# Kernel optimization log

Measured on AMD Instinct MI355X. Metric: run time of the kernel, lower is better.

## Reference

```python
import jax, jax.numpy as jnp
import numpy as np


def setup_inputs() -> dict:
    key = jax.random.key(0)
    k1, k2, k3, k4, k5, k6 = jax.random.split(key, 6)
    B, N, C, H = 4096, 64, 192, 6
    NW = 64  # windows per image; must divide B
    TABLE = 225  # (2*8-1)**2
    qkv = jax.random.normal(k1, (B, N, 3 * C), dtype=jnp.float32)
    rpi = jax.random.randint(k2, (N, N), 0, TABLE, dtype=jnp.int64)
    mask = jax.random.normal(k3, (NW, N, N), dtype=jnp.float32)
    rpb_table = jax.random.normal(k4, (TABLE, H), dtype=jnp.float32) * 0.02
    proj_w = jax.random.normal(k5, (C, C), dtype=jnp.float32) * 0.02
    proj_b = jax.random.normal(k6, (C,), dtype=jnp.float32) * 0.02
    return {"qkv": qkv, "rpi": rpi, "mask": mask, "rpb_table": rpb_table,
            "proj_w": proj_w, "proj_b": proj_b}


def reference(qkv, rpi, mask, rpb_table, proj_w, proj_b):
    b_, n, c3 = qkv.shape
    c = c3 // 3
    h = rpb_table.shape[1]           # num_heads
    hd = c // h                      # head_dim
    scale = hd ** (-0.5)
    # (b_, n, 3, h, hd) -> (3, b_, h, n, hd)
    qkv = qkv.reshape(b_, n, 3, h, hd).transpose(2, 0, 3, 1, 4)
    q, k, v = qkv[0] * scale, qkv[1], qkv[2]
    # windowed QK^T: [b_, h, n, n]
    attn = jnp.einsum('bhqd,bhkd->bhqk', q, k)
    # relative position bias gather: rpi [n,n] -> [h,n,n]
    bias = rpb_table[rpi].transpose(2, 0, 1)
    attn = attn + bias[None]
    # shift-window mask add
    nw = mask.shape[0]
    attn = attn.reshape(b_ // nw, nw, h, n, n) + mask[None, :, None]
    attn = attn.reshape(b_, h, n, n)
    attn = jax.nn.softmax(attn, axis=-1)
    # AV then output projection
    out = jnp.einsum('bhqk,bhkd->bhqd', attn, v)
    out = out.transpose(0, 2, 1, 3).reshape(b_, n, c)
    return out @ proj_w.T + proj_b
```

## Files before the change

kernel.cpp:

```cpp
#include <hip/hip_runtime.h>
#include <stdint.h>

typedef __bf16 bf16x8 __attribute__((ext_vector_type(8)));
typedef float f32x4 __attribute__((ext_vector_type(4)));

__device__ __forceinline__ unsigned short f2bf(float f) {
    union { __bf16 h; unsigned short u; } v;
    v.h = (__bf16)f;
    return v.u;
}
__device__ __forceinline__ float bf2f(unsigned short u) {
    union { uint32_t u32; float f; } v;
    v.u32 = ((uint32_t)u) << 16;
    return v.f;
}

#define QS_STRIDE 40
#define VT_STRIDE 72
#define PS_STRIDE 72
#define XS_STRIDE 200

__global__ void prep_all(const int* __restrict__ rpi32,
                         const float* __restrict__ rpb,
                         const float* __restrict__ proj_w,
                         unsigned short* __restrict__ rpbT,
                         unsigned short* __restrict__ wf) {
    int bid = blockIdx.x;
    int tid = threadIdx.x;
    if (bid < 96) {
        __shared__ int is64_s;
        if (tid == 0) {
            int s = 0;
            #pragma unroll
            for (int i = 0; i < 16; ++i) s |= rpi32[2 * i + 1];
            is64_s = (s == 0);
        }
        __syncthreads();
        int g = bid * 256 + tid;
        int e = g & 4095;
        int h = g >> 12;
        int rv = is64_s ? rpi32[2 * e] : rpi32[e];
        rpbT[g] = f2bf(rpb[rv * 6 + h]);
    } else {
        int g = (bid - 96) * 256 + tid;
        int e = g & 7;
        int lane = (g >> 3) & 63;
        int kkct = g >> 9;
        int kk = kkct / 12, ct = kkct % 12;
        int co = ct * 16 + (lane & 15);
        int ki = kk * 32 + (lane >> 4) * 8 + e;
        wf[g] = f2bf(proj_w[co * 192 + ki]);
    }
}


__global__ __launch_bounds__(256, 3)
void winattn_fast(const float* __restrict__ qkv,
                  const float* __restrict__ mask,
                  const unsigned short* __restrict__ rpbT,
                  const unsigned short* __restrict__ wf,
                  const float* __restrict__ proj_b,
                  float* __restrict__ out) {
    __shared__ __align__(16) unsigned short x_s[64 * XS_STRIDE];
    __shared__ __align__(16) unsigned short u_s[7424];
    __shared__ __align__(16) unsigned short p_s[4 * 16 * PS_STRIDE];

    unsigned short* q_s  = u_s;
    unsigned short* k_s  = u_s + 2560;
    unsigned short* vT_s = u_s + 5120;

    const int tid  = threadIdx.x;
    const int b    = blockIdx.x;
    const int lane = tid & 63;
    const int wv   = tid >> 6;
    const int l16  = lane & 15;
    const int lhi  = lane >> 4;
    const int qbase = wv * 16;
    const float scale = 0.17677669529663687f;

    const float* qkv_b = qkv + (size_t)b * 64 * 576;
    const float* mask_l = mask + (size_t)(b & 63) * 4096 + (qbase + l16) * 64 + lhi * 4;
    const unsigned short* rpb_l = rpbT + (qbase + l16) * 64 + lhi * 4;

    const int tokA = tid >> 3;
    const int dA   = (tid & 7) << 2;
    const float4* gA = (const float4*)(qkv_b + tokA * 576 + dA);
    const float4* gB = (const float4*)(qkv_b + (tokA + 32) * 576 + dA);

    float4 q0, k0, v0, q1, k1, v1;

#define LOADH(h_)  do { int o = (h_) * 8;                         \
        q0 = gA[o];      k0 = gA[o + 48]; v0 = gA[o + 96];        \
        q1 = gB[o];      k1 = gB[o + 48]; v1 = gB[o + 96]; } while (0)

#define STOREH() do {                                             \
        ushort4 qh, kh;                                           \
        qh.x = f2bf(q0.x * scale); qh.y = f2bf(q0.y * scale);     \
        qh.z = f2bf(q0.z * scale); qh.w = f2bf(q0.w * scale);     \
        kh.x = f2bf(k0.x); kh.y = f2bf(k0.y);                     \
        kh.z = f2bf(k0.z); kh.w = f2bf(k0.w);                     \
        *(ushort4*)&q_s[tokA * QS_STRIDE + dA] = qh;              \
        *(ushort4*)&k_s[tokA * QS_STRIDE + dA] = kh;              \
        vT_s[(dA + 0) * VT_STRIDE + tokA] = f2bf(v0.x);           \
        vT_s[(dA + 1) * VT_STRIDE + tokA] = f2bf(v0.y);           \
        vT_s[(dA + 2) * VT_STRIDE + tokA] = f2bf(v0.z);           \
        vT_s[(dA + 3) * VT_STRIDE + tokA] = f2bf(v0.w);           \
        qh.x = f2bf(q1.x * scale); qh.y = f2bf(q1.y * scale);     \
        qh.z = f2bf(q1.z * scale); qh.w = f2bf(q1.w * scale);     \
        kh.x = f2bf(k1.x); kh.y = f2bf(k1.y);                     \
        kh.z = f2bf(k1.z); kh.w = f2bf(k1.w);                     \
        *(ushort4*)&q_s[(tokA + 32) * QS_STRIDE + dA] = qh;       \
        *(ushort4*)&k_s[(tokA + 32) * QS_STRIDE + dA] = kh;       \
        vT_s[(dA + 0) * VT_STRIDE + tokA + 32] = f2bf(v1.x);      \
        vT_s[(dA + 1) * VT_STRIDE + tokA + 32] = f2bf(v1.y);      \
        vT_s[(dA + 2) * VT_STRIDE + tokA + 32] = f2bf(v1.z);      \
        vT_s[(dA + 3) * VT_STRIDE + tokA + 32] = f2bf(v1.w); } while (0)

    LOADH(0);
    STOREH();

    unsigned short* pw = p_s + wv * 16 * PS_STRIDE;

    float4 mv[4];
    #pragma unroll
    for (int nt = 0; nt < 4; ++nt)
        mv[nt] = *(const float4*)&mask_l[nt * 16];
    ushort4 rb[4], rbn[4];
    #pragma unroll
    for (int nt = 0; nt < 4; ++nt)
        rb[nt] = *(const ushort4*)&rpb_l[nt * 16];

    for (int h = 0; h < 6; ++h) {
        __syncthreads();
        if (h < 5) {
            LOADH(h + 1);
            #pragma unroll
            for (int nt = 0; nt < 4; ++nt)
                rbn[nt] = *(const ushort4*)&rpb_l[(h + 1) * 4096 + nt * 16];
        }

        float bias[4][4];
        #pragma unroll
        for (int nt = 0; nt < 4; ++nt) {
            bias[nt][0] = mv[nt].x + bf2f(rb[nt].x);
            bias[nt][1] = mv[nt].y + bf2f(rb[nt].y);
            bias[nt][2] = mv[nt].z + bf2f(rb[nt].z);
            bias[nt][3] = mv[nt].w + bf2f(rb[nt].w);
        }

        bf16x8 aq = *(const bf16x8*)&q_s[(qbase + l16) * QS_STRIDE + lhi * 8];
        float lg[4][4];
        #pragma unroll
        for (int nt = 0; nt < 4; ++nt) {
            bf16x8 bk = *(const bf16x8*)&k_s[(nt * 16 + l16) * QS_STRIDE + lhi * 8];
            f32x4 c = {0.f, 0.f, 0.f, 0.f};
            c = __builtin_amdgcn_mfma_f32_16x16x32_bf16(bk, aq, c, 0, 0, 0);
            lg[nt][0] = c[0] + bias[nt][0]; lg[nt][1] = c[1] + bias[nt][1];
            lg[nt][2] = c[2] + bias[nt][2]; lg[nt][3] = c[3] + bias[nt][3];
        }

        float m = lg[0][0];
        #pragma unroll
        for (int nt = 0; nt < 4; ++nt)
            #pragma unroll
            for (int j = 0; j < 4; ++j) m = fmaxf(m, lg[nt][j]);
        m = fmaxf(m, __shfl_xor(m, 16, 64));
        m = fmaxf(m, __shfl_xor(m, 32, 64));
        float s = 0.f;
        #pragma unroll
        for (int nt = 0; nt < 4; ++nt)
            #pragma unroll
            for (int j = 0; j < 4; ++j) { lg[nt][j] = __expf(lg[nt][j] - m); s += lg[nt][j]; }
        s += __shfl_xor(s, 16, 64);
        s += __shfl_xor(s, 32, 64);
        float inv = __builtin_amdgcn_rcpf(s);

        #pragma unroll
        for (int nt = 0; nt < 4; ++nt) {
            ushort4 ph;
            ph.x = f2bf(lg[nt][0] * inv); ph.y = f2bf(lg[nt][1] * inv);
            ph.z = f2bf(lg[nt][2] * inv); ph.w = f2bf(lg[nt][3] * inv);
            *(ushort4*)&pw[l16 * PS_STRIDE + nt * 16 + lhi * 4] = ph;
        }

        f32x4 xo[2] = {{0.f,0.f,0.f,0.f},{0.f,0.f,0.f,0.f}};
        #pragma unroll
        for (int kk = 0; kk < 2; ++kk) {
            bf16x8 pa = *(const bf16x8*)&pw[l16 * PS_STRIDE + kk * 32 + lhi * 8];
            #pragma unroll
            for (int dt = 0; dt < 2; ++dt) {
                bf16x8 vb = *(const bf16x8*)&vT_s[(dt * 16 + l16) * VT_STRIDE + kk * 32 + lhi * 8];
                xo[dt] = __builtin_amdgcn_mfma_f32_16x16x32_bf16(pa, vb, xo[dt], 0, 0, 0);
            }
        }
        #pragma unroll
        for (int j = 0; j < 4; ++j) {
            int n = qbase + lhi * 4 + j;
            #pragma unroll
            for (int dt = 0; dt < 2; ++dt)
                x_s[n * XS_STRIDE + h * 32 + dt * 16 + l16] = f2bf(xo[dt][j]);
        }

        __syncthreads();
        if (h < 5) {
            STOREH();
            #pragma unroll
            for (int nt = 0; nt < 4; ++nt) rb[nt] = rbn[nt];
        }
    }
#undef LOADH
#undef STOREH

    f32x4 oacc[12];
    #pragma unroll
    for (int ct = 0; ct < 12; ++ct) oacc[ct] = (f32x4){0.f, 0.f, 0.f, 0.f};
    #pragma unroll
    for (int kk = 0; kk < 6; ++kk) {
        bf16x8 ax = *(const bf16x8*)&x_s[(qbase + l16) * XS_STRIDE + kk * 32 + lhi * 8];
        #pragma unroll
        for (int ct = 0; ct < 12; ++ct) {
            bf16x8 bw = *(const bf16x8*)&wf[((kk * 12 + ct) * 64 + lane) * 8];
            oacc[ct] = __builtin_amdgcn_mfma_f32_16x16x32_bf16(ax, bw, oacc[ct], 0, 0, 0);
        }
    }
    float* outb = out + (size_t)b * 64 * 192;
    #pragma unroll
    for (int ct = 0; ct < 12; ++ct) {
        int co = ct * 16 + l16;
        float bias = proj_b[co];
        #pragma unroll
        for (int j = 0; j < 4; ++j) {
            int n = qbase + lhi * 4 + j;
            outb[n * 192 + co] = oacc[ct][j] + bias;
        }
    }
}


#define WS_STRIDE 40

__global__ __launch_bounds__(256)
void winattn_fused(const float* __restrict__ qkv,
                   const int* __restrict__ rpi32,
                   const float* __restrict__ mask,
                   const float* __restrict__ rpb_table,
                   const float* __restrict__ proj_w,
                   const float* __restrict__ proj_b,
                   float* __restrict__ out) {
    __shared__ __align__(16) unsigned short x_s[64 * XS_STRIDE];
    __shared__ __align__(16) unsigned short u_s[12032];
    __shared__ float rpb_s[225];
    __shared__ int rpi_is64_s;

    unsigned short* q_s  = u_s;
    unsigned short* k_s  = u_s + 2560;
    unsigned short* vT_s = u_s + 5120;
    unsigned short* p_s  = u_s + 7424;
    unsigned short* w_s  = u_s;

    const int tid  = threadIdx.x;
    const int b    = blockIdx.x;
    const int lane = tid & 63;
    const int wv   = tid >> 6;
    const int l16  = lane & 15;
    const int lhi  = lane >> 4;
    const int qbase = wv * 16;
    const float scale = 0.17677669529663687f;

    if (tid == 0) {
        int s = 0;
        #pragma unroll
        for (int i = 0; i < 16; ++i) s |= rpi32[2 * i + 1];
        rpi_is64_s = (s == 0) ? 1 : 0;
    }

    const float* maskw = mask + (size_t)(b & 63) * 4096;
    const float* qkv_b = qkv + (size_t)b * 64 * 576;

    for (int h = 0; h < 6; ++h) {
        for (int idx = tid; idx < 64 * 8; idx += 256) {
            int tok = idx >> 3, d = (idx & 7) << 2;
            const float4* base = (const float4*)(qkv_b + tok * 576 + h * 32 + d);
            float4 qv = base[0];
            float4 kv = base[48];
            float4 vv = base[96];
            ushort4 qh, kh;
            qh.x = f2bf(qv.x * scale); qh.y = f2bf(qv.y * scale);
            qh.z = f2bf(qv.z * scale); qh.w = f2bf(qv.w * scale);
            kh.x = f2bf(kv.x); kh.y = f2bf(kv.y); kh.z = f2bf(kv.z); kh.w = f2bf(kv.w);
            *(ushort4*)&q_s[tok * QS_STRIDE + d] = qh;
            *(ushort4*)&k_s[tok * QS_STRIDE + d] = kh;
            vT_s[(d + 0) * VT_STRIDE + tok] = f2bf(vv.x);
            vT_s[(d + 1) * VT_STRIDE + tok] = f2bf(vv.y);
            vT_s[(d + 2) * VT_STRIDE + tok] = f2bf(vv.z);
            vT_s[(d + 3) * VT_STRIDE + tok] = f2bf(vv.w);
        }
        if (tid < 225) rpb_s[tid] = rpb_table[tid * 6 + h];
        __syncthreads();
        const int is64 = rpi_is64_s;

        bf16x8 aq = *(const bf16x8*)&q_s[(qbase + l16) * QS_STRIDE + lhi * 8];
        float lg[4][4];
        #pragma unroll
        for (int nt = 0; nt < 4; ++nt) {
            bf16x8 bk = *(const bf16x8*)&k_s[(nt * 16 + l16) * QS_STRIDE + lhi * 8];
            f32x4 c = {0.f, 0.f, 0.f, 0.f};
            c = __builtin_amdgcn_mfma_f32_16x16x32_bf16(aq, bk, c, 0, 0, 0);
            #pragma unroll
            for (int j = 0; j < 4; ++j) lg[nt][j] = c[j];
        }
        #pragma unroll
        for (int nt = 0; nt < 4; ++nt) {
            int c = nt * 16 + l16;
            #pragma unroll
            for (int j = 0; j < 4; ++j) {
                int r = qbase + lhi * 4 + j;
                int e = r * 64 + c;
                int rv = is64 ? rpi32[2 * e] : rpi32[e];
                lg[nt][j] += rpb_s[rv] + maskw[e];
            }
        }
        float srow[4];
        float p[4][4];
        #pragma unroll
        for (int j = 0; j < 4; ++j) {
            float m = fmaxf(fmaxf(lg[0][j], lg[1][j]), fmaxf(lg[2][j], lg[3][j]));
            #pragma unroll
            for (int o = 1; o < 16; o <<= 1) m = fmaxf(m, __shfl_xor(m, o, 64));
            float s = 0.f;
            #pragma unroll
            for (int nt = 0; nt < 4; ++nt) { p[nt][j] = __expf(lg[nt][j] - m); s += p[nt][j]; }
            #pragma unroll
            for (int o = 1; o < 16; o <<= 1) s += __shfl_xor(s, o, 64);
            srow[j] = s;
        }
        __syncthreads();
        unsigned short* pw = p_s + wv * 16 * PS_STRIDE;
        #pragma unroll
        for (int nt = 0; nt < 4; ++nt)
            #pragma unroll
            for (int j = 0; j < 4; ++j)
                pw[(lhi * 4 + j) * PS_STRIDE + nt * 16 + l16] = f2bf(p[nt][j]);
        __syncthreads();

        f32x4 xo[2] = {{0.f,0.f,0.f,0.f},{0.f,0.f,0.f,0.f}};
        #pragma unroll
        for (int kk = 0; kk < 2; ++kk) {
            bf16x8 pa = *(const bf16x8*)&pw[l16 * PS_STRIDE + kk * 32 + lhi * 8];
            #pragma unroll
            for (int dt = 0; dt < 2; ++dt) {
                bf16x8 vb = *(const bf16x8*)&vT_s[(dt * 16 + l16) * VT_STRIDE + kk * 32 + lhi * 8];
                xo[dt] = __builtin_amdgcn_mfma_f32_16x16x32_bf16(pa, vb, xo[dt], 0, 0, 0);
            }
        }
        #pragma unroll
        for (int j = 0; j < 4; ++j) {
            float inv = 1.f / srow[j];
            int n = qbase + lhi * 4 + j;
            #pragma unroll
            for (int dt = 0; dt < 2; ++dt)
                x_s[n * XS_STRIDE + h * 32 + dt * 16 + l16] = f2bf(xo[dt][j] * inv);
        }
        __syncthreads();
    }

    f32x4 oacc[12];
    #pragma unroll
    for (int ct = 0; ct < 12; ++ct) oacc[ct] = (f32x4){0.f, 0.f, 0.f, 0.f};
    for (int kk = 0; kk < 6; ++kk) {
        for (int idx = tid; idx < 192 * 8; idx += 256) {
            int co = idx >> 3, d = (idx & 7) << 2;
            float4 wvv = *(const float4*)(proj_w + co * 192 + kk * 32 + d);
            ushort4 wh;
            wh.x = f2bf(wvv.x); wh.y = f2bf(wvv.y); wh.z = f2bf(wvv.z); wh.w = f2bf(wvv.w);
            *(ushort4*)&w_s[co * WS_STRIDE + d] = wh;
        }
        __syncthreads();
        bf16x8 ax = *(const bf16x8*)&x_s[(qbase + l16) * XS_STRIDE + kk * 32 + lhi * 8];
        #pragma unroll
        for (int ct = 0; ct < 12; ++ct) {
            bf16x8 bw = *(const bf16x8*)&w_s[(ct * 16 + l16) * WS_STRIDE + lhi * 8];
            oacc[ct] = __builtin_amdgcn_mfma_f32_16x16x32_bf16(ax, bw, oacc[ct], 0, 0, 0);
        }
        __syncthreads();
    }
    float* outb = out + (size_t)b * 64 * 192;
    #pragma unroll
    for (int ct = 0; ct < 12; ++ct) {
        int co = ct * 16 + l16;
        float bias = proj_b[co];
        #pragma unroll
        for (int j = 0; j < 4; ++j) {
            int n = qbase + lhi * 4 + j;
            outb[n * 192 + co] = oacc[ct][j] + bias;
        }
    }
}

extern "C" void kernel_launch(void* const* d_in, const int* in_sizes, int n_in,
                              void* d_out, int out_size, void* d_ws, size_t ws_size,
                              hipStream_t stream) {
    (void)in_sizes; (void)n_in; (void)out_size;
    const float* qkv       = (const float*)d_in[0];
    const int*   rpi       = (const int*)d_in[1];
    const float* mask      = (const float*)d_in[2];
    const float* rpb_table = (const float*)d_in[3];
    const float* proj_w    = (const float*)d_in[4];
    const float* proj_b    = (const float*)d_in[5];
    float* out = (float*)d_out;

    const size_t RT_BYTES = (size_t)6 * 4096 * sizeof(unsigned short);
    const size_t WF_BYTES = (size_t)36864 * sizeof(unsigned short);

    if (ws_size >= RT_BYTES + WF_BYTES) {
        unsigned short* rpbT = (unsigned short*)d_ws;
        unsigned short* wfp  = (unsigned short*)((char*)d_ws + RT_BYTES);
        prep_all<<<240, 256, 0, stream>>>(rpi, rpb_table, proj_w, rpbT, wfp);
        winattn_fast<<<4096, 256, 0, stream>>>(qkv, mask, rpbT, wfp, proj_b, out);
    } else {
        winattn_fused<<<4096, 256, 0, stream>>>(qkv, rpi, mask, rpb_table, proj_w, proj_b, out);
    }
}
```

Measured before the change: 186.7 us.

## Double-buffer per-head QKV tiles and keep attention outputs in registers

The per-head q/k/vT shared tile is now double-buffered. That removes the second __syncthreads per head, and the global load for head h+2 is issued one iteration earlier. The full 64x192 bf16 x_s staging buffer is replaced by a small per-wave 16x32 scratch. Each head's A-fragment for the output projection is read back right away and held in six bf16x8 registers. This lowers LDS footprint and barrier count, at the cost of more live registers under launch_bounds(256,3).

```diff
diff --git a/kernel.cpp b/kernel.cpp
--- a/kernel.cpp
+++ b/kernel.cpp
@@ -18,7 +18,7 @@
 #define QS_STRIDE 40
 #define VT_STRIDE 72
 #define PS_STRIDE 72
-#define XS_STRIDE 200
+#define XH_STRIDE 40
 
 __global__ void prep_all(const int* __restrict__ rpi32,
                          const float* __restrict__ rpb,
@@ -61,13 +61,9 @@
                   const unsigned short* __restrict__ wf,
                   const float* __restrict__ proj_b,
                   float* __restrict__ out) {
-    __shared__ __align__(16) unsigned short x_s[64 * XS_STRIDE];
-    __shared__ __align__(16) unsigned short u_s[7424];
+    __shared__ __align__(16) unsigned short u_s[2][7424];
     __shared__ __align__(16) unsigned short p_s[4 * 16 * PS_STRIDE];
-
-    unsigned short* q_s  = u_s;
-    unsigned short* k_s  = u_s + 2560;
-    unsigned short* vT_s = u_s + 5120;
+    __shared__ __align__(16) unsigned short xh_s[4 * 16 * XH_STRIDE];
 
     const int tid  = threadIdx.x;
     const int b    = blockIdx.x;
@@ -93,33 +89,38 @@
         q0 = gA[o];      k0 = gA[o + 48]; v0 = gA[o + 96];        \
         q1 = gB[o];      k1 = gB[o + 48]; v1 = gB[o + 96]; } while (0)
 
-#define STOREH() do {                                             \
+#define STOREH(buf) do {                                          \
+        unsigned short* q_w  = (buf);                             \
+        unsigned short* k_w  = (buf) + 2560;                      \
+        unsigned short* vT_w = (buf) + 5120;                      \
         ushort4 qh, kh;                                           \
         qh.x = f2bf(q0.x * scale); qh.y = f2bf(q0.y * scale);     \
         qh.z = f2bf(q0.z * scale); qh.w = f2bf(q0.w * scale);     \
         kh.x = f2bf(k0.x); kh.y = f2bf(k0.y);                     \
         kh.z = f2bf(k0.z); kh.w = f2bf(k0.w);                     \
-        *(ushort4*)&q_s[tokA * QS_STRIDE + dA] = qh;              \
-        *(ushort4*)&k_s[tokA * QS_STRIDE + dA] = kh;              \
-        vT_s[(dA + 0) * VT_STRIDE + tokA] = f2bf(v0.x);           \
-        vT_s[(dA + 1) * VT_STRIDE + tokA] = f2bf(v0.y);           \
-        vT_s[(dA + 2) * VT_STRIDE + tokA] = f2bf(v0.z);           \
-        vT_s[(dA + 3) * VT_STRIDE + tokA] = f2bf(v0.w);           \
+        *(ushort4*)&q_w[tokA * QS_STRIDE + dA] = qh;              \
+        *(ushort4*)&k_w[tokA * QS_STRIDE + dA] = kh;              \
+        vT_w[(dA + 0) * VT_STRIDE + tokA] = f2bf(v0.x);           \
+        vT_w[(dA + 1) * VT_STRIDE + tokA] = f2bf(v0.y);           \
+        vT_w[(dA + 2) * VT_STRIDE + tokA] = f2bf(v0.z);           \
+        vT_w[(dA + 3) * VT_STRIDE + tokA] = f2bf(v0.w);           \
         qh.x = f2bf(q1.x * scale); qh.y = f2bf(q1.y * scale);     \
         qh.z = f2bf(q1.z * scale); qh.w = f2bf(q1.w * scale);     \
         kh.x = f2bf(k1.x); kh.y = f2bf(k1.y);                     \
         kh.z = f2bf(k1.z); kh.w = f2bf(k1.w);                     \
-        *(ushort4*)&q_s[(tokA + 32) * QS_STRIDE + dA] = qh;       \
-        *(ushort4*)&k_s[(tokA + 32) * QS_STRIDE + dA] = kh;       \
-        vT_s[(dA + 0) * VT_STRIDE + tokA + 32] = f2bf(v1.x);      \
-        vT_s[(dA + 1) * VT_STRIDE + tokA + 32] = f2bf(v1.y);      \
-        vT_s[(dA + 2) * VT_STRIDE + tokA + 32] = f2bf(v1.z);      \
-        vT_s[(dA + 3) * VT_STRIDE + tokA + 32] = f2bf(v1.w); } while (0)
+        *(ushort4*)&q_w[(tokA + 32) * QS_STRIDE + dA] = qh;       \
+        *(ushort4*)&k_w[(tokA + 32) * QS_STRIDE + dA] = kh;       \
+        vT_w[(dA + 0) * VT_STRIDE + tokA + 32] = f2bf(v1.x);      \
+        vT_w[(dA + 1) * VT_STRIDE + tokA + 32] = f2bf(v1.y);      \
+        vT_w[(dA + 2) * VT_STRIDE + tokA + 32] = f2bf(v1.z);      \
+        vT_w[(dA + 3) * VT_STRIDE + tokA + 32] = f2bf(v1.w); } while (0)
 
     LOADH(0);
-    STOREH();
+    STOREH(u_s[0]);
+    LOADH(1);
 
     unsigned short* pw = p_s + wv * 16 * PS_STRIDE;
+    unsigned short* xh = xh_s + wv * 16 * XH_STRIDE;
 
     float4 mv[4];
     #pragma unroll
@@ -130,14 +131,19 @@
     for (int nt = 0; nt < 4; ++nt)
         rb[nt] = *(const ushort4*)&rpb_l[nt * 16];
 
+    bf16x8 ax0, ax1, ax2, ax3, ax4, ax5;
+
+    #pragma unroll
     for (int h = 0; h < 6; ++h) {
         __syncthreads();
         if (h < 5) {
-            LOADH(h + 1);
             #pragma unroll
             for (int nt = 0; nt < 4; ++nt)
                 rbn[nt] = *(const ushort4*)&rpb_l[(h + 1) * 4096 + nt * 16];
         }
+        const unsigned short* q_s  = u_s[h & 1];
+        const unsigned short* k_s  = u_s[h & 1] + 2560;
+        const unsigned short* vT_s = u_s[h & 1] + 5120;
 
         float bias[4][4];
         #pragma unroll
@@ -195,15 +201,23 @@
         }
         #pragma unroll
         for (int j = 0; j < 4; ++j) {
-            int n = qbase + lhi * 4 + j;
             #pragma unroll
             for (int dt = 0; dt < 2; ++dt)
-                x_s[n * XS_STRIDE + h * 32 + dt * 16 + l16] = f2bf(xo[dt][j]);
-        }
-
-        __syncthreads();
+                xh[(lhi * 4 + j) * XH_STRIDE + dt * 16 + l16] = f2bf(xo[dt][j]);
+        }
+        {
+            bf16x8 axv = *(const bf16x8*)&xh[l16 * XH_STRIDE + lhi * 8];
+            if (h == 0) ax0 = axv;
+            else if (h == 1) ax1 = axv;
+            else if (h == 2) ax2 = axv;
+            else if (h == 3) ax3 = axv;
+            else if (h == 4) ax4 = axv;
+            else             ax5 = axv;
+        }
+
         if (h < 5) {
-            STOREH();
+            STOREH(u_s[(h + 1) & 1]);
+            if (h < 4) LOADH(h + 2);
             #pragma unroll
             for (int nt = 0; nt < 4; ++nt) rb[nt] = rbn[nt];
         }
@@ -216,7 +230,8 @@
     for (int ct = 0; ct < 12; ++ct) oacc[ct] = (f32x4){0.f, 0.f, 0.f, 0.f};
     #pragma unroll
     for (int kk = 0; kk < 6; ++kk) {
-        bf16x8 ax = *(const bf16x8*)&x_s[(qbase + l16) * XS_STRIDE + kk * 32 + lhi * 8];
+        bf16x8 ax = (kk == 0) ? ax0 : (kk == 1) ? ax1 : (kk == 2) ? ax2
+                  : (kk == 3) ? ax3 : (kk == 4) ? ax4 : ax5;
         #pragma unroll
         for (int ct = 0; ct < 12; ++ct) {
             bf16x8 bw = *(const bf16x8*)&wf[((kk * 12 + ct) * 64 + lane) * 8];
@@ -237,6 +252,7 @@
 }
 
 
+#define XS_STRIDE 200
 #define WS_STRIDE 40
 
 __global__ __launch_bounds__(256)
```

Result: slower. 196.9 us (+5.5%).
